# Kernel optimization log

Hardware: AMD Instinct MI355X
Metric: run time of the kernel (lower is better)

Reference implementation:

```python
import jax, jax.numpy as jnp
import numpy as np

H = 8      # num_attention_heads
DH = 96    # attention_head_size
LN_EPS = 1e-5


def setup_inputs() -> dict:
    key = jax.random.key(0)
    ks = jax.random.split(key, 12)
    B, S, D = 2, 768, 768
    sc = 0.02
    return {
        "hidden_states": jax.random.normal(ks[0], (B, S, D), jnp.float32),
        "distance_matrix": jax.random.uniform(ks[1], (B, S, S), jnp.float32) * 20.0,
        "angle_matrix": jax.random.uniform(ks[2], (B, S, S), jnp.float32) * np.pi,
        "attention_mask": jnp.ones((B, S), jnp.float32),
        "Wq": jax.random.normal(ks[3], (D, D), jnp.float32) * sc,
        "bq": jnp.zeros((D,), jnp.float32),
        "Wk": jax.random.normal(ks[4], (D, D), jnp.float32) * sc,
        "bk": jnp.zeros((D,), jnp.float32),
        "Wv": jax.random.normal(ks[5], (D, D), jnp.float32) * sc,
        "bv": jnp.zeros((D,), jnp.float32),
        "Wd": jax.random.normal(ks[6], (DH,), jnp.float32) * sc,
        "bd": jnp.zeros((DH,), jnp.float32),
        "Wa": jax.random.normal(ks[7], (DH,), jnp.float32) * sc,
        "ba": jnp.zeros((DH,), jnp.float32),
        "Wo": jax.random.normal(ks[8], (D, D), jnp.float32) * sc,
        "bo": jnp.zeros((D,), jnp.float32),
        "ln_g": jnp.ones((D,), jnp.float32),
        "ln_b": jnp.zeros((D,), jnp.float32),
    }


def _heads(x, B, S):
    # [B,S,D] -> [B,H,S,DH]
    return x.reshape(B, S, H, DH).transpose(0, 2, 1, 3)


def reference(hidden_states, distance_matrix, angle_matrix, attention_mask,
              Wq, bq, Wk, bk, Wv, bv, Wd, bd, Wa, ba, Wo, bo, ln_g, ln_b):
    B, S, D = hidden_states.shape
    q = _heads(hidden_states @ Wq.T + bq, B, S)   # [B,H,S,DH]
    k = _heads(hidden_states @ Wk.T + bk, B, S)
    v = _heads(hidden_states @ Wv.T + bv, B, S)

    scores = jnp.einsum('bhid,bhjd->bhij', q, k) / jnp.sqrt(jnp.float32(DH))

    # distance / angle relative-position biases: emb[b,i,j,:] = dist[b,i,j]*Wd + bd
    dist_emb = distance_matrix[..., None] * Wd + bd   # [B,S,S,DH]
    scores = scores + jnp.einsum('bhid,bijd->bhij', q, dist_emb)
    ang_emb = angle_matrix[..., None] * Wa + ba       # [B,S,S,DH]
    scores = scores + jnp.einsum('bhid,bijd->bhij', q, ang_emb)

    # key mask, broadcast over heads and query positions
    scores = scores + (1.0 - attention_mask)[:, None, None, :] * -10000.0

    probs = jax.nn.softmax(scores, axis=-1)           # [B,H,S,S]
    ctx = jnp.einsum('bhij,bhjd->bhid', probs, v)
    ctx = ctx.transpose(0, 2, 1, 3).reshape(B, S, D)  # [B,S,D]

    out = ctx @ Wo.T + bo
    x = out + hidden_states
    mu = jnp.mean(x, axis=-1, keepdims=True)
    var = jnp.var(x, axis=-1, keepdims=True)
    out = (x - mu) * jax.lax.rsqrt(var + LN_EPS) * ln_g + ln_b
    return out, probs
```

## Files before the change

### kernel.cpp

```cpp
#include <hip/hip_runtime.h>
#include <stdint.h>

#define B_  2
#define S_  768
#define D_  768
#define H_  8
#define DH_ 96

typedef unsigned short ushort_t;
typedef __bf16 bf16x8 __attribute__((ext_vector_type(8)));
typedef float  f32x4  __attribute__((ext_vector_type(4)));

__device__ inline ushort_t f2bf(float f) {
    union { float f; unsigned int u; } v; v.f = f;
    unsigned int u = v.u;
    unsigned int r = u + 0x7fffu + ((u >> 16) & 1u);
    return (ushort_t)(r >> 16);
}
__device__ inline float bf2f(ushort_t u) {
    union { unsigned int i; float f; } c; c.i = ((unsigned int)u) << 16;
    return c.f;
}

__device__ inline void glds16(const void* gp, void* lp) {
    auto g = reinterpret_cast<const __attribute__((address_space(1))) uint32_t*>(
        reinterpret_cast<uintptr_t>(gp));
    auto l = reinterpret_cast<__attribute__((address_space(3))) uint32_t*>(
        reinterpret_cast<uintptr_t>(lp));
    __builtin_amdgcn_global_load_lds(g, l, 16, 0, 0);
}

__global__ __launch_bounds__(256) void k_convert(
        const float* __restrict__ X, const float* __restrict__ Wq,
        const float* __restrict__ Wk, const float* __restrict__ Wv,
        const float* __restrict__ Wo,
        ushort_t* __restrict__ Xb, ushort_t* __restrict__ Wb) {
    const int NX4 = (B_ * S_ * D_) / 4;
    const int NW4 = (D_ * D_) / 4;
    int i = blockIdx.x * blockDim.x + threadIdx.x;
    float4 v;
    ushort_t* dst;
    if (i < NX4) {
        v = ((const float4*)X)[i];
        dst = Xb + i * 4;
    } else {
        int wi = i - NX4;
        int sel = wi / NW4;
        int off = wi - sel * NW4;
        const float* src = (sel == 0) ? Wq : (sel == 1) ? Wk : (sel == 2) ? Wv : Wo;
        v = ((const float4*)src)[off];
        dst = Wb + wi * 4;
    }
    ushort4 o;
    o.x = f2bf(v.x); o.y = f2bf(v.y); o.z = f2bf(v.z); o.w = f2bf(v.w);
    *(ushort4*)dst = o;
}

__device__ inline void gemm64_glds(
        const ushort_t* __restrict__ A, int lda,
        const ushort_t* __restrict__ Bt, int ldb,
        int K, int m0, int n0,
        ushort_t* As, ushort_t* Bs, f32x4 acc[2][2]) {
    const int tid  = threadIdx.x;
    const int lane = tid & 63, wave = tid >> 6;
    const int wm = (wave >> 1) * 32, wn = (wave & 1) * 32;
    const int fr = lane & 15, fk = (lane >> 4) * 8;
    const int sr = wave * 16 + (lane >> 2);
    const int sc = (lane & 3) * 8;
    const ushort_t* Ap = A  + (size_t)(m0 + sr) * lda + sc;
    const ushort_t* Bp = Bt + (size_t)(n0 + sr) * ldb + sc;
    ushort_t* AsW = As + wave * 512;
    ushort_t* BsW = Bs + wave * 512;
    for (int kt = 0; kt < K; kt += 32) {
        if (kt) __syncthreads();
        glds16(Ap + kt, AsW);
        glds16(Bp + kt, BsW);
        __syncthreads();
        bf16x8 a0 = *(const bf16x8*)&As[(wm      + fr) * 32 + fk];
        bf16x8 a1 = *(const bf16x8*)&As[(wm + 16 + fr) * 32 + fk];
        bf16x8 b0 = *(const bf16x8*)&Bs[(wn      + fr) * 32 + fk];
        bf16x8 b1 = *(const bf16x8*)&Bs[(wn + 16 + fr) * 32 + fk];
        acc[0][0] = __builtin_amdgcn_mfma_f32_16x16x32_bf16(a0, b0, acc[0][0], 0, 0, 0);
        acc[0][1] = __builtin_amdgcn_mfma_f32_16x16x32_bf16(a0, b1, acc[0][1], 0, 0, 0);
        acc[1][0] = __builtin_amdgcn_mfma_f32_16x16x32_bf16(a1, b0, acc[1][0], 0, 0, 0);
        acc[1][1] = __builtin_amdgcn_mfma_f32_16x16x32_bf16(a1, b1, acc[1][1], 0, 0, 0);
    }
}

__global__ __launch_bounds__(256) void k_qkv(
        const ushort_t* __restrict__ Xb, const ushort_t* __restrict__ Wb,
        const float* __restrict__ bq, const float* __restrict__ bk,
        const float* __restrict__ bv,
        ushort_t* __restrict__ Qb, ushort_t* __restrict__ Kb,
        ushort_t* __restrict__ Vtb) {
    __shared__ __align__(16) ushort_t As[64 * 32];
    __shared__ __align__(16) ushort_t Bs[64 * 32];
    f32x4 acc[2][2];
    #pragma unroll
    for (int i = 0; i < 2; i++)
        #pragma unroll
        for (int j = 0; j < 2; j++) acc[i][j] = (f32x4){0.f, 0.f, 0.f, 0.f};
    const int m0 = blockIdx.y * 64, n0 = blockIdx.x * 64;
    gemm64_glds(Xb, D_, Wb, D_, D_, m0, n0, As, Bs, acc);
    const int lane = threadIdx.x & 63, wave = threadIdx.x >> 6;
    const int wm = (wave >> 1) * 32, wn = (wave & 1) * 32;
    #pragma unroll
    for (int ni = 0; ni < 2; ni++) {
        int gcol = n0 + wn + ni * 16 + (lane & 15);
        int g = gcol / D_, d768 = gcol - g * D_;
        int h = d768 / DH_, d = d768 - h * DH_;
        float bias = (g == 0 ? bq : (g == 1 ? bk : bv))[d768];
        #pragma unroll
        for (int mi = 0; mi < 2; mi++) {
            #pragma unroll
            for (int r = 0; r < 4; r++) {
                int grow = m0 + wm + mi * 16 + (lane >> 4) * 4 + r;
                int b = grow / S_, s = grow - b * S_;
                ushort_t ob = f2bf(acc[mi][ni][r] + bias);
                int bh = b * H_ + h;
                if (g == 0)      Qb[((size_t)bh * S_ + s) * DH_ + d] = ob;
                else if (g == 1) Kb[((size_t)bh * S_ + s) * DH_ + d] = ob;
                else             Vtb[((size_t)bh * DH_ + d) * S_ + s] = ob;
            }
        }
    }
}

__global__ __launch_bounds__(256) void k_qcoef(
        const ushort_t* __restrict__ Qb,
        const float* __restrict__ Wd, const float* __restrict__ bd,
        const float* __restrict__ Wa, const float* __restrict__ ba,
        float* __restrict__ qcoef) {
    const int wave = threadIdx.x >> 6, lane = threadIdx.x & 63;
    const int row = blockIdx.x * 4 + wave;
    const ushort_t* q = Qb + (size_t)row * DH_;
    float e0 = bf2f(q[lane]);
    float c0 = e0 * Wd[lane];
    float c1 = e0 * Wa[lane];
    float c2 = e0 * (bd[lane] + ba[lane]);
    if (lane < 32) {
        int d = 64 + lane;
        float e1 = bf2f(q[d]);
        c0 += e1 * Wd[d];
        c1 += e1 * Wa[d];
        c2 += e1 * (bd[d] + ba[d]);
    }
    #pragma unroll
    for (int o = 32; o > 0; o >>= 1) {
        c0 += __shfl_down(c0, o);
        c1 += __shfl_down(c1, o);
        c2 += __shfl_down(c2, o);
    }
    if (lane == 0) {
        qcoef[row * 3 + 0] = c0;
        qcoef[row * 3 + 1] = c1;
        qcoef[row * 3 + 2] = c2;
    }
}

#define L1B 29696
__global__ __launch_bounds__(256) void k_flash(
        const ushort_t* __restrict__ Qb, const ushort_t* __restrict__ Kb,
        const ushort_t* __restrict__ Vtb, const float* __restrict__ qcoef,
        const float* __restrict__ distm, const float* __restrict__ angm,
        const float* __restrict__ mask,
        float* __restrict__ probs, ushort_t* __restrict__ Ctxb) {
    __shared__ __align__(16) char sm[2 * L1B + 640];
    float* mstat = (float*)(sm + 2 * L1B);
    float* lstat = (float*)(sm + 2 * L1B + 256);
    float* linv  = (float*)(sm + 2 * L1B + 512);
    const int idx = blockIdx.x;
    const int h = idx / 48, rem = idx - h * 48;
    const int b = rem / 24, r0 = (rem - b * 24) * 32;
    const int bh = b * H_ + h;
    const int tid = threadIdx.x, lane = tid & 63, w = tid >> 6;
    const int frn = lane & 15, fko = (lane >> 4) * 8, frg4 = (lane >> 4) * 4;
    const int rg = w & 1, cp = w >> 1;
    const ushort_t* Qbh = Qb + (size_t)bh * S_ * DH_;
    const ushort_t* Kbh = Kb + (size_t)bh * S_ * DH_;
    const ushort_t* Vbh = Vtb + (size_t)bh * DH_ * S_;

    bf16x8 aq[3];
    {
        const ushort_t* qp = Qbh + (size_t)(r0 + rg * 16 + frn) * DH_ + fko;
        aq[0] = *(const bf16x8*)qp;
        aq[1] = *(const bf16x8*)(qp + 32);
        aq[2] = *(const bf16x8*)(qp + 64);
    }
    float qc0[4], qc1[4], qc2[4];
    #pragma unroll
    for (int r = 0; r < 4; r++) {
        const float* qp = qcoef + ((size_t)bh * S_ + r0 + rg * 16 + frg4 + r) * 3;
        qc0[r] = qp[0]; qc1[r] = qp[1]; qc2[r] = qp[2];
    }
    const float isq = 0.10206207261596577f;

    f32x4 acc[24];
    #pragma unroll
    for (int c = 0; c < 12; ++c) {
        char* bufc = sm + (c & 1) * L1B;
        ushort_t* Ks = (ushort_t*)bufc;
        float* Dd = (float*)(bufc + 12288);
        float* Da = (float*)(bufc + 20992);
        #pragma unroll
        for (int k = 0; k < 3; ++k) {
            int i = tid + 256 * k;
            int row = i / 12, cc = (i - row * 12) * 8;
            *(uint4*)(Ks + row * 96 + cc) =
                *(const uint4*)(Kbh + (size_t)(c * 64 + row) * DH_ + cc);
        }
        #pragma unroll
        for (int k = 0; k < 2; ++k) {
            int i = tid + 256 * k;
            int row = i >> 4, c4 = (i & 15) * 4;
            size_t src = ((size_t)b * S_ + r0 + row) * S_ + c * 64 + c4;
            *(float4*)(Dd + row * 68 + c4) = *(const float4*)(distm + src);
            *(float4*)(Da + row * 68 + c4) = *(const float4*)(angm + src);
        }
        __syncthreads();
        #pragma unroll
        for (int tt = 0; tt < 2; ++tt) {
            const ushort_t* kp = Ks + (cp * 32 + tt * 16 + frn) * 96 + fko;
            f32x4 ca = (f32x4){0.f, 0.f, 0.f, 0.f};
            ca = __builtin_amdgcn_mfma_f32_16x16x32_bf16(aq[0], *(const bf16x8*)kp, ca, 0, 0, 0);
            ca = __builtin_amdgcn_mfma_f32_16x16x32_bf16(aq[1], *(const bf16x8*)(kp + 32), ca, 0, 0, 0);
            ca = __builtin_amdgcn_mfma_f32_16x16x32_bf16(aq[2], *(const bf16x8*)(kp + 64), ca, 0, 0, 0);
            int jl = cp * 32 + tt * 16 + frn;
            float mb = (1.0f - mask[b * S_ + c * 64 + jl]) * -10000.0f;
            #pragma unroll
            for (int r = 0; r < 4; ++r) {
                int rl = rg * 16 + frg4 + r;
                acc[c * 2 + tt][r] = ca[r] * isq + Dd[rl * 68 + jl] * qc0[r]
                                   + Da[rl * 68 + jl] * qc1[r] + qc2[r] + mb;
            }
        }
    }
    float mx[4] = {-1e30f, -1e30f, -1e30f, -1e30f};
    #pragma unroll
    for (int t = 0; t < 24; t++)
        #pragma unroll
        for (int r = 0; r < 4; r++) mx[r] = fmaxf(mx[r], acc[t][r]);
    #pragma unroll
    for (int o = 1; o < 16; o <<= 1)
        #pragma unroll
        for (int r = 0; r < 4; r++) mx[r] = fmaxf(mx[r], __shfl_xor(mx[r], o));
    if (frn == 0)
        #pragma unroll
        for (int r = 0; r < 4; r++) mstat[cp * 32 + rg * 16 + frg4 + r] = mx[r];
    __syncthreads();
    float mf[4], sum[4] = {0.f, 0.f, 0.f, 0.f};
    #pragma unroll
    for (int r = 0; r < 4; r++) {
        int rl = rg * 16 + frg4 + r;
        mf[r] = fmaxf(mstat[rl], mstat[32 + rl]);
    }
    #pragma unroll
    for (int t = 0; t < 24; t++)
        #pragma unroll
        for (int r = 0; r < 4; r++) {
            float e = __expf(acc[t][r] - mf[r]);
            acc[t][r] = e;
            sum[r] += e;
        }
    #pragma unroll
    for (int o = 1; o < 16; o <<= 1)
        #pragma unroll
        for (int r = 0; r < 4; r++) sum[r] += __shfl_xor(sum[r], o);
    if (frn == 0)
        #pragma unroll
        for (int r = 0; r < 4; r++) lstat[cp * 32 + rg * 16 + frg4 + r] = sum[r];
    __syncthreads();
    float inv[4];
    #pragma unroll
    for (int r = 0; r < 4; r++) {
        int rl = rg * 16 + frg4 + r;
        inv[r] = 1.0f / (lstat[rl] + lstat[32 + rl]);
        if (cp == 0 && frn == 0) linv[rl] = inv[r];
    }
    __syncthreads();
    f32x4 accO[3];
    #pragma unroll
    for (int i = 0; i < 3; i++) accO[i] = (f32x4){0.f, 0.f, 0.f, 0.f};
    const int prow = tid >> 3, pc8 = (tid & 7) * 4;
    float* pout = probs + ((size_t)bh * S_ + r0 + prow) * S_;
    const int vrow = tid >> 2, vcv = (tid & 3) * 8;
    const int vrow2 = (tid + 256) >> 2, vcv2 = ((tid + 256) & 3) * 8;
    #pragma unroll
    for (int s = 0; s < 24; ++s) {
        ushort_t* Vs = (ushort_t*)(sm + (s & 1) * 7680);
        ushort_t* Ps = (ushort_t*)(sm + 15360 + (s & 1) * 2560);
        *(uint4*)(Vs + vrow * 40 + vcv) =
            *(const uint4*)(Vbh + (size_t)vrow * S_ + s * 32 + vcv);
        if (tid + 256 < 384)
            *(uint4*)(Vs + vrow2 * 40 + vcv2) =
                *(const uint4*)(Vbh + (size_t)vrow2 * S_ + s * 32 + vcv2);
        if (cp == (s & 1)) {
            #pragma unroll
            for (int tt = 0; tt < 2; ++tt)
                #pragma unroll
                for (int r = 0; r < 4; ++r)
                    Ps[(rg * 16 + frg4 + r) * 40 + tt * 16 + frn] =
                        f2bf(acc[(s & ~1) + tt][r]);
        }
        __syncthreads();
        {
            float iv = linv[prow];
            float4 p4;
            p4.x = bf2f(Ps[prow * 40 + pc8 + 0]) * iv;
            p4.y = bf2f(Ps[prow * 40 + pc8 + 1]) * iv;
            p4.z = bf2f(Ps[prow * 40 + pc8 + 2]) * iv;
            p4.w = bf2f(Ps[prow * 40 + pc8 + 3]) * iv;
            *(float4*)(pout + s * 32 + pc8) = p4;
        }
        bf16x8 a = *(const bf16x8*)&Ps[(rg * 16 + frn) * 40 + fko];
        #pragma unroll
        for (int nt = 0; nt < 3; ++nt) {
            bf16x8 v = *(const bf16x8*)&Vs[(cp * 48 + nt * 16 + frn) * 40 + fko];
            accO[nt] = __builtin_amdgcn_mfma_f32_16x16x32_bf16(a, v, accO[nt], 0, 0, 0);
        }
    }
    #pragma unroll
    for (int nt = 0; nt < 3; ++nt) {
        int col = h * DH_ + cp * 48 + nt * 16 + frn;
        #pragma unroll
        for (int r = 0; r < 4; ++r) {
            int row = r0 + rg * 16 + frg4 + r;
            Ctxb[((size_t)(b * S_ + row)) * D_ + col] = f2bf(accO[nt][r] * inv[r]);
        }
    }
}

__global__ __launch_bounds__(256) void k_out(
        const ushort_t* __restrict__ Ctxb, const ushort_t* __restrict__ Wob,
        const float* __restrict__ bo, const float* __restrict__ hidden,
        float* __restrict__ xbuf) {
    __shared__ __align__(16) ushort_t As[64 * 32];
    __shared__ __align__(16) ushort_t Bs[64 * 32];
    f32x4 acc[2][2];
    #pragma unroll
    for (int i = 0; i < 2; i++)
        #pragma unroll
        for (int j = 0; j < 2; j++) acc[i][j] = (f32x4){0.f, 0.f, 0.f, 0.f};
    const int m0 = blockIdx.y * 64, n0 = blockIdx.x * 64;
    gemm64_glds(Ctxb, D_, Wob, D_, D_, m0, n0, As, Bs, acc);
    const int lane = threadIdx.x & 63, wave = threadIdx.x >> 6;
    const int wm = (wave >> 1) * 32, wn = (wave & 1) * 32;
    #pragma unroll
    for (int ni = 0; ni < 2; ni++) {
        int gcol = n0 + wn + ni * 16 + (lane & 15);
        float bias = bo[gcol];
        #pragma unroll
        for (int mi = 0; mi < 2; mi++) {
            #pragma unroll
            for (int r = 0; r < 4; r++) {
                int grow = m0 + wm + mi * 16 + (lane >> 4) * 4 + r;
                xbuf[(size_t)grow * D_ + gcol] =
                    acc[mi][ni][r] + bias + hidden[(size_t)grow * D_ + gcol];
            }
        }
    }
}

__global__ __launch_bounds__(256) void k_ln(
        const float* __restrict__ xbuf, const float* __restrict__ g,
        const float* __restrict__ bb, float* __restrict__ out) {
    const float* x = xbuf + (size_t)blockIdx.x * D_;
    const int t = threadIdx.x;
    float a0 = x[t], a1 = x[t + 256], a2 = x[t + 512];
    float s = a0 + a1 + a2;
    float ss = a0 * a0 + a1 * a1 + a2 * a2;
    __shared__ float r1[4], r2[4];
    #pragma unroll
    for (int o = 32; o > 0; o >>= 1) { s += __shfl_down(s, o); ss += __shfl_down(ss, o); }
    if ((t & 63) == 0) { r1[t >> 6] = s; r2[t >> 6] = ss; }
    __syncthreads();
    float ts = r1[0] + r1[1] + r1[2] + r1[3];
    float tss = r2[0] + r2[1] + r2[2] + r2[3];
    float mu = ts * (1.0f / D_);
    float var = tss * (1.0f / D_) - mu * mu;
    float rstd = rsqrtf(var + 1e-5f);
    float* o = out + (size_t)blockIdx.x * D_;
    o[t]       = (a0 - mu) * rstd * g[t]       + bb[t];
    o[t + 256] = (a1 - mu) * rstd * g[t + 256] + bb[t + 256];
    o[t + 512] = (a2 - mu) * rstd * g[t + 512] + bb[t + 512];
}

extern "C" void kernel_launch(void* const* d_in, const int* in_sizes, int n_in,
                              void* d_out, int out_size, void* d_ws, size_t ws_size,
                              hipStream_t stream) {
    const float* X     = (const float*)d_in[0];
    const float* distm = (const float*)d_in[1];
    const float* angm  = (const float*)d_in[2];
    const float* mask  = (const float*)d_in[3];
    const float* Wq    = (const float*)d_in[4];
    const float* bq    = (const float*)d_in[5];
    const float* Wk    = (const float*)d_in[6];
    const float* bk    = (const float*)d_in[7];
    const float* Wv    = (const float*)d_in[8];
    const float* bv    = (const float*)d_in[9];
    const float* Wd    = (const float*)d_in[10];
    const float* bd    = (const float*)d_in[11];
    const float* Wa    = (const float*)d_in[12];
    const float* ba    = (const float*)d_in[13];
    const float* Wo    = (const float*)d_in[14];
    const float* bo    = (const float*)d_in[15];
    const float* ln_g  = (const float*)d_in[16];
    const float* ln_b  = (const float*)d_in[17];

    float* outp  = (float*)d_out;
    float* probs = (float*)d_out + (size_t)B_ * S_ * D_;

    char* ws = (char*)d_ws;
    ushort_t* Xb    = (ushort_t*)(ws + 0);
    ushort_t* Wb    = (ushort_t*)(ws + 2359296);
    ushort_t* Qb    = (ushort_t*)(ws + 7077888);
    ushort_t* Kb    = (ushort_t*)(ws + 9437184);
    ushort_t* Vtb   = (ushort_t*)(ws + 11796480);
    ushort_t* Ctxb  = (ushort_t*)(ws + 14155776);
    float*    qcoef = (float*)   (ws + 16515072);
    float*    xbuf  = (float*)   (ws + 16662528);

    k_convert<<<3456, 256, 0, stream>>>(X, Wq, Wk, Wv, Wo, Xb, Wb);
    k_qkv<<<dim3(36, 24), 256, 0, stream>>>(Xb, Wb, bq, bk, bv, Qb, Kb, Vtb);
    k_qcoef<<<3072, 256, 0, stream>>>(Qb, Wd, bd, Wa, ba, qcoef);
    k_flash<<<384, 256, 0, stream>>>(Qb, Kb, Vtb, qcoef, distm, angm, mask, probs, Ctxb);
    k_out<<<dim3(12, 24), 256, 0, stream>>>(Ctxb, Wb + (size_t)2304 * 768, bo, X, xbuf);
    k_ln<<<1536, 256, 0, stream>>>(xbuf, ln_g, ln_b, outp);
}
```

Before: 179.3 us.

## Double-buffer GEMM tiles and restructure attention kernel with 16-row blocks and async staging

The shared GEMM helper now double-buffers its LDS tiles, so the next K-slice is prefetched while the current one feeds the MFMAs. The QKV epilogue writes V^T as packed 4-element stores. The flash kernel is restructured: each block handles 16 query rows, giving twice as many blocks with an occupancy hint. K, distance and angle tiles are staged asynchronously through swizzled LDS with a one-chunk-ahead prefetch, and P·V reads V directly from global memory, with per-wave partial context sums reduced through LDS atomics. This aims at more parallelism and overlap of loads with compute, at the cost of extra global V traffic and atomic reductions.

```diff
diff --git a/kernel.cpp b/kernel.cpp
--- a/kernel.cpp
+++ b/kernel.cpp
@@ -56,7 +56,7 @@
     *(ushort4*)dst = o;
 }
 
-__device__ inline void gemm64_glds(
+__device__ inline void gemm64_dbuf(
         const ushort_t* __restrict__ A, int lda,
         const ushort_t* __restrict__ Bt, int ldb,
         int K, int m0, int n0,
@@ -65,21 +65,23 @@
     const int lane = tid & 63, wave = tid >> 6;
     const int wm = (wave >> 1) * 32, wn = (wave & 1) * 32;
     const int fr = lane & 15, fk = (lane >> 4) * 8;
-    const int sr = wave * 16 + (lane >> 2);
-    const int sc = (lane & 3) * 8;
-    const ushort_t* Ap = A  + (size_t)(m0 + sr) * lda + sc;
-    const ushort_t* Bp = Bt + (size_t)(n0 + sr) * ldb + sc;
-    ushort_t* AsW = As + wave * 512;
-    ushort_t* BsW = Bs + wave * 512;
+    const ushort_t* Ap = A  + (size_t)(m0 + wave * 16 + (lane >> 2)) * lda + (lane & 3) * 8;
+    const ushort_t* Bp = Bt + (size_t)(n0 + wave * 16 + (lane >> 2)) * ldb + (lane & 3) * 8;
+    glds16(Ap, As + wave * 512);
+    glds16(Bp, Bs + wave * 512);
     for (int kt = 0; kt < K; kt += 32) {
-        if (kt) __syncthreads();
-        glds16(Ap + kt, AsW);
-        glds16(Bp + kt, BsW);
+        const int cur = (kt >> 5) & 1;
         __syncthreads();
-        bf16x8 a0 = *(const bf16x8*)&As[(wm      + fr) * 32 + fk];
-        bf16x8 a1 = *(const bf16x8*)&As[(wm + 16 + fr) * 32 + fk];
-        bf16x8 b0 = *(const bf16x8*)&Bs[(wn      + fr) * 32 + fk];
-        bf16x8 b1 = *(const bf16x8*)&Bs[(wn + 16 + fr) * 32 + fk];
+        if (kt + 32 < K) {
+            glds16(Ap + kt + 32, As + (cur ^ 1) * 2048 + wave * 512);
+            glds16(Bp + kt + 32, Bs + (cur ^ 1) * 2048 + wave * 512);
+        }
+        const ushort_t* Ab = As + cur * 2048;
+        const ushort_t* Bb = Bs + cur * 2048;
+        bf16x8 a0 = *(const bf16x8*)&Ab[(wm      + fr) * 32 + fk];
+        bf16x8 a1 = *(const bf16x8*)&Ab[(wm + 16 + fr) * 32 + fk];
+        bf16x8 b0 = *(const bf16x8*)&Bb[(wn      + fr) * 32 + fk];
+        bf16x8 b1 = *(const bf16x8*)&Bb[(wn + 16 + fr) * 32 + fk];
         acc[0][0] = __builtin_amdgcn_mfma_f32_16x16x32_bf16(a0, b0, acc[0][0], 0, 0, 0);
         acc[0][1] = __builtin_amdgcn_mfma_f32_16x16x32_bf16(a0, b1, acc[0][1], 0, 0, 0);
         acc[1][0] = __builtin_amdgcn_mfma_f32_16x16x32_bf16(a1, b0, acc[1][0], 0, 0, 0);
@@ -93,34 +95,42 @@
         const float* __restrict__ bv,
         ushort_t* __restrict__ Qb, ushort_t* __restrict__ Kb,
         ushort_t* __restrict__ Vtb) {
-    __shared__ __align__(16) ushort_t As[64 * 32];
-    __shared__ __align__(16) ushort_t Bs[64 * 32];
+    __shared__ __align__(16) ushort_t As[2 * 64 * 32];
+    __shared__ __align__(16) ushort_t Bs[2 * 64 * 32];
     f32x4 acc[2][2];
     #pragma unroll
     for (int i = 0; i < 2; i++)
         #pragma unroll
         for (int j = 0; j < 2; j++) acc[i][j] = (f32x4){0.f, 0.f, 0.f, 0.f};
     const int m0 = blockIdx.y * 64, n0 = blockIdx.x * 64;
-    gemm64_glds(Xb, D_, Wb, D_, D_, m0, n0, As, Bs, acc);
+    gemm64_dbuf(Xb, D_, Wb, D_, D_, m0, n0, As, Bs, acc);
     const int lane = threadIdx.x & 63, wave = threadIdx.x >> 6;
     const int wm = (wave >> 1) * 32, wn = (wave & 1) * 32;
     #pragma unroll
     for (int ni = 0; ni < 2; ni++) {
         int gcol = n0 + wn + ni * 16 + (lane & 15);
-        int g = gcol / D_, d768 = gcol - g * D_;
+        int gsel = gcol / D_, d768 = gcol - gsel * D_;
         int h = d768 / DH_, d = d768 - h * DH_;
-        float bias = (g == 0 ? bq : (g == 1 ? bk : bv))[d768];
+        float bias = (gsel == 0 ? bq : (gsel == 1 ? bk : bv))[d768];
         #pragma unroll
         for (int mi = 0; mi < 2; mi++) {
-            #pragma unroll
-            for (int r = 0; r < 4; r++) {
-                int grow = m0 + wm + mi * 16 + (lane >> 4) * 4 + r;
-                int b = grow / S_, s = grow - b * S_;
-                ushort_t ob = f2bf(acc[mi][ni][r] + bias);
-                int bh = b * H_ + h;
-                if (g == 0)      Qb[((size_t)bh * S_ + s) * DH_ + d] = ob;
-                else if (g == 1) Kb[((size_t)bh * S_ + s) * DH_ + d] = ob;
-                else             Vtb[((size_t)bh * DH_ + d) * S_ + s] = ob;
+            int grow0 = m0 + wm + mi * 16 + (lane >> 4) * 4;
+            int b = grow0 / S_, s0 = grow0 - b * S_;
+            int bh = b * H_ + h;
+            if (gsel == 2) {
+                ushort4 o4;
+                o4.x = f2bf(acc[mi][ni][0] + bias);
+                o4.y = f2bf(acc[mi][ni][1] + bias);
+                o4.z = f2bf(acc[mi][ni][2] + bias);
+                o4.w = f2bf(acc[mi][ni][3] + bias);
+                *(ushort4*)&Vtb[((size_t)bh * DH_ + d) * S_ + s0] = o4;
+            } else {
+                #pragma unroll
+                for (int r = 0; r < 4; r++) {
+                    ushort_t ob = f2bf(acc[mi][ni][r] + bias);
+                    if (gsel == 0) Qb[((size_t)bh * S_ + s0 + r) * DH_ + d] = ob;
+                    else           Kb[((size_t)bh * S_ + s0 + r) * DH_ + d] = ob;
+                }
             }
         }
     }
@@ -158,175 +168,164 @@
     }
 }
 
-#define L1B 29696
-__global__ __launch_bounds__(256) void k_flash(
+#define FL1B 20480
+__global__ __launch_bounds__(256, 3) void k_flash(
         const ushort_t* __restrict__ Qb, const ushort_t* __restrict__ Kb,
         const ushort_t* __restrict__ Vtb, const float* __restrict__ qcoef,
         const float* __restrict__ distm, const float* __restrict__ angm,
         const float* __restrict__ mask,
         float* __restrict__ probs, ushort_t* __restrict__ Ctxb) {
-    __shared__ __align__(16) char sm[2 * L1B + 640];
-    float* mstat = (float*)(sm + 2 * L1B);
-    float* lstat = (float*)(sm + 2 * L1B + 256);
-    float* linv  = (float*)(sm + 2 * L1B + 512);
+    __shared__ __align__(16) char sm[2 * FL1B + 512];
+    float* mstat = (float*)(sm + 2 * FL1B);
+    float* lstat = (float*)(sm + 2 * FL1B + 256);
     const int idx = blockIdx.x;
-    const int h = idx / 48, rem = idx - h * 48;
-    const int b = rem / 24, r0 = (rem - b * 24) * 32;
+    const int h = idx / 96, rem = idx - h * 96;
+    const int b = rem / 48, r0 = (rem - b * 48) * 16;
     const int bh = b * H_ + h;
     const int tid = threadIdx.x, lane = tid & 63, w = tid >> 6;
-    const int frn = lane & 15, fko = (lane >> 4) * 8, frg4 = (lane >> 4) * 4;
-    const int rg = w & 1, cp = w >> 1;
+    const int frn = lane & 15, g = lane >> 4;
     const ushort_t* Qbh = Qb + (size_t)bh * S_ * DH_;
     const ushort_t* Kbh = Kb + (size_t)bh * S_ * DH_;
     const ushort_t* Vbh = Vtb + (size_t)bh * DH_ * S_;
 
-    bf16x8 aq[3];
+    auto stage = [&](int c) {
+        char* bufc = sm + (c & 1) * FL1B;
+        ushort_t* Ks = (ushort_t*)bufc;
+        const ushort_t* kg = Kbh + (size_t)c * 64 * DH_;
+        #pragma unroll
+        for (int t = 0; t < 3; ++t) {
+            int grp = w * 3 + t;
+            glds16(kg + (size_t)lane * DH_ + grp * 8, Ks + grp * 512);
+        }
+        int row = 4 * w + g;
+        int colb = (frn ^ (row & 7)) << 2;
+        size_t src = ((size_t)b * S_ + r0 + row) * S_ + c * 64 + colb;
+        glds16(distm + src, (float*)(bufc + 12288) + w * 256);
+        glds16(angm  + src, (float*)(bufc + 16384) + w * 256);
+    };
+
+    stage(0);
+
+    bf16x8 aq0, aq1, aq2;
     {
-        const ushort_t* qp = Qbh + (size_t)(r0 + rg * 16 + frn) * DH_ + fko;
-        aq[0] = *(const bf16x8*)qp;
-        aq[1] = *(const bf16x8*)(qp + 32);
-        aq[2] = *(const bf16x8*)(qp + 64);
-    }
-    float qc0[4], qc1[4], qc2[4];
-    #pragma unroll
-    for (int r = 0; r < 4; r++) {
-        const float* qp = qcoef + ((size_t)bh * S_ + r0 + rg * 16 + frg4 + r) * 3;
-        qc0[r] = qp[0]; qc1[r] = qp[1]; qc2[r] = qp[2];
+        const ushort_t* qp = Qbh + (size_t)(r0 + frn) * DH_ + g * 8;
+        aq0 = *(const bf16x8*)qp;
+        aq1 = *(const bf16x8*)(qp + 32);
+        aq2 = *(const bf16x8*)(qp + 64);
+    }
+    float qc0, qc1, qc2;
+    {
+        const float* qp = qcoef + ((size_t)bh * S_ + r0 + frn) * 3;
+        qc0 = qp[0]; qc1 = qp[1]; qc2 = qp[2];
     }
     const float isq = 0.10206207261596577f;
-
-    f32x4 acc[24];
+    const int dswz = ((4 * w + g) ^ (frn & 7)) << 2;
+    const int jrow = (16 * w + frn) * 8;
+
+    f32x4 acc[12];
+    __syncthreads();
     #pragma unroll
     for (int c = 0; c < 12; ++c) {
-        char* bufc = sm + (c & 1) * L1B;
-        ushort_t* Ks = (ushort_t*)bufc;
-        float* Dd = (float*)(bufc + 12288);
-        float* Da = (float*)(bufc + 20992);
-        #pragma unroll
-        for (int k = 0; k < 3; ++k) {
-            int i = tid + 256 * k;
-            int row = i / 12, cc = (i - row * 12) * 8;
-            *(uint4*)(Ks + row * 96 + cc) =
-                *(const uint4*)(Kbh + (size_t)(c * 64 + row) * DH_ + cc);
-        }
-        #pragma unroll
-        for (int k = 0; k < 2; ++k) {
-            int i = tid + 256 * k;
-            int row = i >> 4, c4 = (i & 15) * 4;
-            size_t src = ((size_t)b * S_ + r0 + row) * S_ + c * 64 + c4;
-            *(float4*)(Dd + row * 68 + c4) = *(const float4*)(distm + src);
-            *(float4*)(Da + row * 68 + c4) = *(const float4*)(angm + src);
-        }
+        if (c < 11) stage(c + 1);
+        char* bufc = sm + (c & 1) * FL1B;
+        const ushort_t* Ks = (const ushort_t*)bufc;
+        const float* Dd = (const float*)(bufc + 12288);
+        const float* Da = (const float*)(bufc + 16384);
+        bf16x8 k0 = *(const bf16x8*)&Ks[(g    ) * 512 + jrow];
+        bf16x8 k1 = *(const bf16x8*)&Ks[(g + 4) * 512 + jrow];
+        bf16x8 k2 = *(const bf16x8*)&Ks[(g + 8) * 512 + jrow];
+        f32x4 ca = (f32x4){0.f, 0.f, 0.f, 0.f};
+        ca = __builtin_amdgcn_mfma_f32_16x16x32_bf16(k0, aq0, ca, 0, 0, 0);
+        ca = __builtin_amdgcn_mfma_f32_16x16x32_bf16(k1, aq1, ca, 0, 0, 0);
+        ca = __builtin_amdgcn_mfma_f32_16x16x32_bf16(k2, aq2, ca, 0, 0, 0);
+        float4 d4 = *(const float4*)(Dd + frn * 64 + dswz);
+        float4 a4 = *(const float4*)(Da + frn * 64 + dswz);
+        float4 m4 = *(const float4*)(mask + b * S_ + c * 64 + w * 16 + g * 4);
+        f32x4 o;
+        o[0] = ca[0] * isq + d4.x * qc0 + a4.x * qc1 + qc2 + (1.f - m4.x) * -10000.f;
+        o[1] = ca[1] * isq + d4.y * qc0 + a4.y * qc1 + qc2 + (1.f - m4.y) * -10000.f;
+        o[2] = ca[2] * isq + d4.z * qc0 + a4.z * qc1 + qc2 + (1.f - m4.z) * -10000.f;
+        o[3] = ca[3] * isq + d4.w * qc0 + a4.w * qc1 + qc2 + (1.f - m4.w) * -10000.f;
+        acc[c] = o;
         __syncthreads();
-        #pragma unroll
-        for (int tt = 0; tt < 2; ++tt) {
-            const ushort_t* kp = Ks + (cp * 32 + tt * 16 + frn) * 96 + fko;
-            f32x4 ca = (f32x4){0.f, 0.f, 0.f, 0.f};
-            ca = __builtin_amdgcn_mfma_f32_16x16x32_bf16(aq[0], *(const bf16x8*)kp, ca, 0, 0, 0);
-            ca = __builtin_amdgcn_mfma_f32_16x16x32_bf16(aq[1], *(const bf16x8*)(kp + 32), ca, 0, 0, 0);
-            ca = __builtin_amdgcn_mfma_f32_16x16x32_bf16(aq[2], *(const bf16x8*)(kp + 64), ca, 0, 0, 0);
-            int jl = cp * 32 + tt * 16 + frn;
-            float mb = (1.0f - mask[b * S_ + c * 64 + jl]) * -10000.0f;
-            #pragma unroll
-            for (int r = 0; r < 4; ++r) {
-                int rl = rg * 16 + frg4 + r;
-                acc[c * 2 + tt][r] = ca[r] * isq + Dd[rl * 68 + jl] * qc0[r]
-                                   + Da[rl * 68 + jl] * qc1[r] + qc2[r] + mb;
-            }
-        }
-    }
-    float mx[4] = {-1e30f, -1e30f, -1e30f, -1e30f};
-    #pragma unroll
-    for (int t = 0; t < 24; t++)
-        #pragma unroll
-        for (int r = 0; r < 4; r++) mx[r] = fmaxf(mx[r], acc[t][r]);
-    #pragma unroll
-    for (int o = 1; o < 16; o <<= 1)
-        #pragma unroll
-        for (int r = 0; r < 4; r++) mx[r] = fmaxf(mx[r], __shfl_xor(mx[r], o));
-    if (frn == 0)
-        #pragma unroll
-        for (int r = 0; r < 4; r++) mstat[cp * 32 + rg * 16 + frg4 + r] = mx[r];
-    __syncthreads();
-    float mf[4], sum[4] = {0.f, 0.f, 0.f, 0.f};
-    #pragma unroll
-    for (int r = 0; r < 4; r++) {
-        int rl = rg * 16 + frg4 + r;
-        mf[r] = fmaxf(mstat[rl], mstat[32 + rl]);
-    }
-    #pragma unroll
-    for (int t = 0; t < 24; t++)
-        #pragma unroll
-        for (int r = 0; r < 4; r++) {
-            float e = __expf(acc[t][r] - mf[r]);
-            acc[t][r] = e;
-            sum[r] += e;
-        }
-    #pragma unroll
-    for (int o = 1; o < 16; o <<= 1)
-        #pragma unroll
-        for (int r = 0; r < 4; r++) sum[r] += __shfl_xor(sum[r], o);
-    if (frn == 0)
-        #pragma unroll
-        for (int r = 0; r < 4; r++) lstat[cp * 32 + rg * 16 + frg4 + r] = sum[r];
-    __syncthreads();
-    float inv[4];
-    #pragma unroll
-    for (int r = 0; r < 4; r++) {
-        int rl = rg * 16 + frg4 + r;
-        inv[r] = 1.0f / (lstat[rl] + lstat[32 + rl]);
-        if (cp == 0 && frn == 0) linv[rl] = inv[r];
-    }
-    __syncthreads();
-    f32x4 accO[3];
-    #pragma unroll
-    for (int i = 0; i < 3; i++) accO[i] = (f32x4){0.f, 0.f, 0.f, 0.f};
-    const int prow = tid >> 3, pc8 = (tid & 7) * 4;
-    float* pout = probs + ((size_t)bh * S_ + r0 + prow) * S_;
-    const int vrow = tid >> 2, vcv = (tid & 3) * 8;
-    const int vrow2 = (tid + 256) >> 2, vcv2 = ((tid + 256) & 3) * 8;
-    #pragma unroll
-    for (int s = 0; s < 24; ++s) {
-        ushort_t* Vs = (ushort_t*)(sm + (s & 1) * 7680);
-        ushort_t* Ps = (ushort_t*)(sm + 15360 + (s & 1) * 2560);
-        *(uint4*)(Vs + vrow * 40 + vcv) =
-            *(const uint4*)(Vbh + (size_t)vrow * S_ + s * 32 + vcv);
-        if (tid + 256 < 384)
-            *(uint4*)(Vs + vrow2 * 40 + vcv2) =
-                *(const uint4*)(Vbh + (size_t)vrow2 * S_ + s * 32 + vcv2);
-        if (cp == (s & 1)) {
-            #pragma unroll
-            for (int tt = 0; tt < 2; ++tt)
-                #pragma unroll
-                for (int r = 0; r < 4; ++r)
-                    Ps[(rg * 16 + frg4 + r) * 40 + tt * 16 + frn] =
-                        f2bf(acc[(s & ~1) + tt][r]);
-        }
-        __syncthreads();
-        {
-            float iv = linv[prow];
-            float4 p4;
-            p4.x = bf2f(Ps[prow * 40 + pc8 + 0]) * iv;
-            p4.y = bf2f(Ps[prow * 40 + pc8 + 1]) * iv;
-            p4.z = bf2f(Ps[prow * 40 + pc8 + 2]) * iv;
-            p4.w = bf2f(Ps[prow * 40 + pc8 + 3]) * iv;
-            *(float4*)(pout + s * 32 + pc8) = p4;
-        }
-        bf16x8 a = *(const bf16x8*)&Ps[(rg * 16 + frn) * 40 + fko];
-        #pragma unroll
-        for (int nt = 0; nt < 3; ++nt) {
-            bf16x8 v = *(const bf16x8*)&Vs[(cp * 48 + nt * 16 + frn) * 40 + fko];
-            accO[nt] = __builtin_amdgcn_mfma_f32_16x16x32_bf16(a, v, accO[nt], 0, 0, 0);
-        }
-    }
-    #pragma unroll
-    for (int nt = 0; nt < 3; ++nt) {
-        int col = h * DH_ + cp * 48 + nt * 16 + frn;
+    }
+
+    float mx = -1e30f;
+    #pragma unroll
+    for (int c = 0; c < 12; ++c)
+        #pragma unroll
+        for (int r = 0; r < 4; ++r) mx = fmaxf(mx, acc[c][r]);
+    mx = fmaxf(mx, __shfl_xor(mx, 16));
+    mx = fmaxf(mx, __shfl_xor(mx, 32));
+    if (g == 0) mstat[w * 16 + frn] = mx;
+    __syncthreads();
+    float mf = fmaxf(fmaxf(mstat[frn], mstat[16 + frn]),
+                     fmaxf(mstat[32 + frn], mstat[48 + frn]));
+    float sum = 0.f;
+    #pragma unroll
+    for (int c = 0; c < 12; ++c)
         #pragma unroll
         for (int r = 0; r < 4; ++r) {
-            int row = r0 + rg * 16 + frg4 + r;
-            Ctxb[((size_t)(b * S_ + row)) * D_ + col] = f2bf(accO[nt][r] * inv[r]);
-        }
+            float e = __expf(acc[c][r] - mf);
+            acc[c][r] = e;
+            sum += e;
+        }
+    sum += __shfl_xor(sum, 16);
+    sum += __shfl_xor(sum, 32);
+    if (g == 0) lstat[w * 16 + frn] = sum;
+    __syncthreads();
+    float inv = 1.f / (lstat[frn] + lstat[16 + frn] + lstat[32 + frn] + lstat[48 + frn]);
+
+    float* ctxred = (float*)sm;
+    {
+        int zr = tid >> 4, zc = tid & 15;
+        #pragma unroll
+        for (int i = 0; i < 6; ++i) ctxred[zr * 100 + i * 16 + zc] = 0.f;
+    }
+    __syncthreads();
+
+    f32x4 accO[6];
+    #pragma unroll
+    for (int i = 0; i < 6; ++i) accO[i] = (f32x4){0.f, 0.f, 0.f, 0.f};
+    float* prow = probs + ((size_t)bh * S_ + r0 + frn) * S_ + w * 16 + g * 4;
+    const ushort_t* vbase = Vbh + (size_t)frn * S_ + w * 16 + g * 4;
+    #pragma unroll
+    for (int c = 0; c < 12; c += 2) {
+        float4 p;
+        p.x = acc[c][0] * inv; p.y = acc[c][1] * inv;
+        p.z = acc[c][2] * inv; p.w = acc[c][3] * inv;
+        *(float4*)(prow + c * 64) = p;
+        p.x = acc[c + 1][0] * inv; p.y = acc[c + 1][1] * inv;
+        p.z = acc[c + 1][2] * inv; p.w = acc[c + 1][3] * inv;
+        *(float4*)(prow + (c + 1) * 64) = p;
+        union { bf16x8 v; ushort_t u[8]; } pa;
+        #pragma unroll
+        for (int r = 0; r < 4; ++r) {
+            pa.u[r]     = f2bf(acc[c][r]);
+            pa.u[r + 4] = f2bf(acc[c + 1][r]);
+        }
+        #pragma unroll
+        for (int nt = 0; nt < 6; ++nt) {
+            const ushort_t* vp = vbase + (size_t)nt * 16 * S_ + c * 64;
+            union { bf16x8 v; uint2 q2[2]; } vb;
+            vb.q2[0] = *(const uint2*)vp;
+            vb.q2[1] = *(const uint2*)(vp + 64);
+            accO[nt] = __builtin_amdgcn_mfma_f32_16x16x32_bf16(pa.v, vb.v, accO[nt], 0, 0, 0);
+        }
+    }
+    #pragma unroll
+    for (int nt = 0; nt < 6; ++nt)
+        #pragma unroll
+        for (int r = 0; r < 4; ++r)
+            atomicAdd(&ctxred[(4 * g + r) * 100 + nt * 16 + frn], accO[nt][r]);
+    __syncthreads();
+    {
+        int zr = tid >> 4, zc = tid & 15;
+        float ivr = 1.f / (lstat[zr] + lstat[16 + zr] + lstat[32 + zr] + lstat[48 + zr]);
+        ushort_t* crow = Ctxb + ((size_t)b * S_ + r0 + zr) * D_ + h * DH_;
+        #pragma unroll
+        for (int i = 0; i < 6; ++i)
+            crow[i * 16 + zc] = f2bf(ctxred[zr * 100 + i * 16 + zc] * ivr);
     }
 }
 
@@ -334,15 +333,15 @@
         const ushort_t* __restrict__ Ctxb, const ushort_t* __restrict__ Wob,
         const float* __restrict__ bo, const float* __restrict__ hidden,
         float* __restrict__ xbuf) {
-    __shared__ __align__(16) ushort_t As[64 * 32];
-    __shared__ __align__(16) ushort_t Bs[64 * 32];
+    __shared__ __align__(16) ushort_t As[2 * 64 * 32];
+    __shared__ __align__(16) ushort_t Bs[2 * 64 * 32];
     f32x4 acc[2][2];
     #pragma unroll
     for (int i = 0; i < 2; i++)
         #pragma unroll
         for (int j = 0; j < 2; j++) acc[i][j] = (f32x4){0.f, 0.f, 0.f, 0.f};
     const int m0 = blockIdx.y * 64, n0 = blockIdx.x * 64;
-    gemm64_glds(Ctxb, D_, Wob, D_, D_, m0, n0, As, Bs, acc);
+    gemm64_dbuf(Ctxb, D_, Wob, D_, D_, m0, n0, As, Bs, acc);
     const int lane = threadIdx.x & 63, wave = threadIdx.x >> 6;
     const int wm = (wave >> 1) * 32, wn = (wave & 1) * 32;
     #pragma unroll
@@ -423,7 +422,7 @@
     k_convert<<<3456, 256, 0, stream>>>(X, Wq, Wk, Wv, Wo, Xb, Wb);
     k_qkv<<<dim3(36, 24), 256, 0, stream>>>(Xb, Wb, bq, bk, bv, Qb, Kb, Vtb);
     k_qcoef<<<3072, 256, 0, stream>>>(Qb, Wd, bd, Wa, ba, qcoef);
-    k_flash<<<384, 256, 0, stream>>>(Qb, Kb, Vtb, qcoef, distm, angm, mask, probs, Ctxb);
+    k_flash<<<768, 256, 0, stream>>>(Qb, Kb, Vtb, qcoef, distm, angm, mask, probs, Ctxb);
     k_out<<<dim3(12, 24), 256, 0, stream>>>(Ctxb, Wb + (size_t)2304 * 768, bo, X, xbuf);
     k_ln<<<1536, 256, 0, stream>>>(xbuf, ln_g, ln_b, outp);
 }
```

New measurement: 207.6 us. 15.7% more time.
